# Kernel tuning notes

Hardware: AMD Instinct MI355X
Metric: run time of the kernel (lower is better)

## Reference

```python
import jax, jax.numpy as jnp
from jax import lax
import numpy as np

T, B, H, NUM_DATA, IN_DIM = 2048, 256, 128, 4096, 1


def setup_inputs() -> dict:
    key = jax.random.key(0)
    ks = jax.random.split(key, 9)
    s = 1.0 / np.sqrt(H)  # PyTorch LSTM/Linear default init scale
    inp = {
        "input": jax.random.normal(ks[0], (T, B, IN_DIM), dtype=jnp.float32),
        "label": jax.random.randint(ks[1], (B,), 0, NUM_DATA),
        "h0": jnp.zeros((1, NUM_DATA, H), dtype=jnp.float32),
        "W_ih": jax.random.uniform(ks[2], (4 * H, IN_DIM), jnp.float32, -s, s),
        "W_hh": jax.random.uniform(ks[3], (4 * H, H), jnp.float32, -s, s),
        "b_ih": jax.random.uniform(ks[4], (4 * H,), jnp.float32, -s, s),
        "b_hh": jax.random.uniform(ks[5], (4 * H,), jnp.float32, -s, s),
        "W_lin": jax.random.uniform(ks[6], (IN_DIM, H), jnp.float32, -s, s),
        "b_lin": jax.random.uniform(ks[7], (IN_DIM,), jnp.float32, -s, s),
    }
    return inp


def reference(input, label, h0, W_ih, W_hh, b_ih, b_hh, W_lin, b_lin):
    seq_len = input.shape[0]
    num_in_batch = input.shape[1]
    # Gather learned initial hidden state per sequence id (the python cat loop in torch)
    h = h0[0, label]                                   # (B, H)
    c = jnp.zeros_like(h)                              # (B, H)
    y0 = jnp.zeros((num_in_batch, IN_DIM), input.dtype)  # t=0 input is zeros
    b = b_ih + b_hh                                    # (4H,)

    def step(carry, _):
        h, c, x = carry
        gates = x @ W_ih.T + h @ W_hh.T + b            # (B, 4H); torch gate order i,f,g,o
        i, f, g, o = jnp.split(gates, 4, axis=-1)
        i = jax.nn.sigmoid(i)
        f = jax.nn.sigmoid(f)
        g = jnp.tanh(g)
        o = jax.nn.sigmoid(o)
        c = f * c + i * g
        h = o * jnp.tanh(c)
        y = h @ W_lin.T + b_lin                        # (B, 1) -> fed back as next input
        return (h, c, y), y

    _, ys = lax.scan(step, (h, c, y0), None, length=seq_len)
    return ys  # (T, B, 1), matches torch cat of (1, B, 1) along dim 0
```

## Files before the change

kernel.cpp:

```cpp
#include <hip/hip_runtime.h>
#include <math.h>

#define T_STEPS 2048
#define BATCH   256
#define HDIM    128

__device__ __forceinline__ float fast_rcp(float x) { return __builtin_amdgcn_rcpf(x); }
__device__ __forceinline__ float sigmoid_f(float x) { return fast_rcp(1.0f + __expf(-x)); }
__device__ __forceinline__ float tanh_f(float x) {
    float e = __expf(2.0f * x);
    return 1.0f - 2.0f * fast_rcp(e + 1.0f);
}

#define REP8(M) M(0) M(1) M(2) M(3) M(4) M(5) M(6) M(7)

__global__ __launch_bounds__(512, 2)
void lstm_seq_kernel(const int*   __restrict__ label,
                     const float* __restrict__ h0,
                     const float* __restrict__ W_ih,
                     const float* __restrict__ W_hh,
                     const float* __restrict__ b_ih,
                     const float* __restrict__ b_hh,
                     const float* __restrict__ W_lin,
                     const float* __restrict__ b_lin,
                     float*       __restrict__ out)
{
    const int tid   = threadIdx.x;
    const int batch = blockIdx.x;
    const int m     = tid >> 2;
    const int q     = tid & 3;
    const int q8    = q * 8;

    const int ri = m, rf = m + 128, rg = m + 256, ro = m + 384;

    __shared__ float hbuf[2][160];
    __shared__ __attribute__((aligned(16))) float hist[128 * 132];

    const float4* W4 = (const float4*)W_hh;
    const float4* L4 = (const float4*)W_lin;

    #define DECL_W(i) \
        float4 wi##i = W4[ri * 32 + q8 + (i)]; \
        float4 wf##i = W4[rf * 32 + q8 + (i)]; \
        float4 wg##i = W4[rg * 32 + q8 + (i)]; \
        float4 wo##i = W4[ro * 32 + q8 + (i)];
    REP8(DECL_W)

    const float wih_i = W_ih[ri], wih_f = W_ih[rf];
    const float wih_g = W_ih[rg], wih_o = W_ih[ro];
    const float blin  = b_lin[0];

    const float bi_ = b_ih[ri] + b_hh[ri] + wih_i * blin;
    const float bf_ = b_ih[rf] + b_hh[rf] + wih_f * blin;
    const float bg_ = b_ih[rg] + b_hh[rg] + wih_g * blin;
    const float bo_ = b_ih[ro] + b_hh[ro] + wih_o * blin;

    const float bi4_ = bi_ * 0.25f;
    const float bf4_ = bf_ * 0.25f;
    const float bg4_ = bg_ * 0.25f;
    const float bo4_ = bo_ * 0.25f;

    #define FOLD_W(i) { float4 lv = L4[q8 + (i)]; \
        wi##i.x = fmaf(wih_i, lv.x, wi##i.x); wi##i.y = fmaf(wih_i, lv.y, wi##i.y); \
        wi##i.z = fmaf(wih_i, lv.z, wi##i.z); wi##i.w = fmaf(wih_i, lv.w, wi##i.w); \
        wf##i.x = fmaf(wih_f, lv.x, wf##i.x); wf##i.y = fmaf(wih_f, lv.y, wf##i.y); \
        wf##i.z = fmaf(wih_f, lv.z, wf##i.z); wf##i.w = fmaf(wih_f, lv.w, wf##i.w); \
        wg##i.x = fmaf(wih_g, lv.x, wg##i.x); wg##i.y = fmaf(wih_g, lv.y, wg##i.y); \
        wg##i.z = fmaf(wih_g, lv.z, wg##i.z); wg##i.w = fmaf(wih_g, lv.w, wg##i.w); \
        wo##i.x = fmaf(wih_o, lv.x, wo##i.x); wo##i.y = fmaf(wih_o, lv.y, wo##i.y); \
        wo##i.z = fmaf(wih_o, lv.z, wo##i.z); wo##i.w = fmaf(wih_o, lv.w, wo##i.w); }
    REP8(FOLD_W)

    const int   lane = tid & 63;
    const int   ya0w = lane + ((lane >> 5) << 2);
    const float wl_a = W_lin[lane];
    const float wl_b = W_lin[lane + 64];
    const int   hword = m + ((m >> 5) << 2);

    if (tid < HDIM) hbuf[0][tid + ((tid >> 5) << 2)] = h0[label[batch] * HDIM + tid];
    __syncthreads();

    float p0 = hbuf[0][ya0w] * wl_a + hbuf[0][ya0w + 72] * wl_b;
    #pragma unroll
    for (int off = 1; off < 64; off <<= 1) p0 += __shfl_xor(p0, off, 64);
    const float y0 = p0 + blin;

    const float cbi = bi_ - wih_i * y0;
    const float cbf = bf_ - wih_f * y0;
    const float cbg = bg_ - wih_g * y0;
    const float cbo = bo_ - wih_o * y0;

    const float4* hq0 = (const float4*)(&hbuf[0][0] + 36 * q);
    float ai = 0.f, af = 0.f, ag = 0.f, ao = 0.f;
    #define DOT4(i) { float4 hv = hq0[(i)]; \
        ai = fmaf(hv.x, wi##i.x, ai); ai = fmaf(hv.y, wi##i.y, ai); \
        ai = fmaf(hv.z, wi##i.z, ai); ai = fmaf(hv.w, wi##i.w, ai); \
        af = fmaf(hv.x, wf##i.x, af); af = fmaf(hv.y, wf##i.y, af); \
        af = fmaf(hv.z, wf##i.z, af); af = fmaf(hv.w, wf##i.w, af); \
        ag = fmaf(hv.x, wg##i.x, ag); ag = fmaf(hv.y, wg##i.y, ag); \
        ag = fmaf(hv.z, wg##i.z, ag); ag = fmaf(hv.w, wg##i.w, ag); \
        ao = fmaf(hv.x, wo##i.x, ao); ao = fmaf(hv.y, wo##i.y, ao); \
        ao = fmaf(hv.z, wo##i.z, ao); ao = fmaf(hv.w, wo##i.w, ao); }
    REP8(DOT4)
    ai += __shfl_xor(ai, 1, 64); af += __shfl_xor(af, 1, 64);
    ag += __shfl_xor(ag, 1, 64); ao += __shfl_xor(ao, 1, 64);
    ai += __shfl_xor(ai, 2, 64); af += __shfl_xor(af, 2, 64);
    ag += __shfl_xor(ag, 2, 64); ao += __shfl_xor(ao, 2, 64);
    const float iv0 = sigmoid_f(ai + cbi);
    const float fv0 = sigmoid_f(af + cbf);
    const float gv0 = tanh_f  (ag + cbg);
    const float ov0 = sigmoid_f(ao + cbo);
    float c = iv0 * gv0;
    const float hn0 = ov0 * tanh_f(c);
    if (q == 0) { hbuf[1][hword] = hn0; hist[m] = hn0; }
    __syncthreads();

    const unsigned ldsA  = (unsigned)(unsigned long long)(&hbuf[0][0]);
    const unsigned histB = (unsigned)(unsigned long long)(&hist[0]);
    const unsigned vR0 = ldsA + 640u + 144u * (unsigned)q;
    const unsigned vW0 = ldsA + 4u * (unsigned)hword;
    const unsigned hW0 = histB + 528u + 4u * (unsigned)m;
    const unsigned fR0 = histB + 528u * (unsigned)m + 128u * (unsigned)q;
    const unsigned jO0 = 1024u * (unsigned)m;
    const unsigned vO0 = 4u * (unsigned)batch;
    const unsigned offI = (unsigned)(ri * 512 + q * 128);
    const unsigned offF = (unsigned)(rf * 512 + q * 128);
    const unsigned offG = (unsigned)(rg * 512 + q * 128);
    const unsigned offO = (unsigned)(ro * 512 + q * 128);
    const unsigned offL = (unsigned)(q * 128);

    asm volatile(
        "v_mov_b32 v220, %[bi]\n\t"
        "v_mov_b32 v221, 0\n\t"
        "v_mov_b32 v222, %[bf]\n\t"
        "v_mov_b32 v223, 0\n\t"
        "v_mov_b32 v224, %[bg]\n\t"
        "v_mov_b32 v225, 0\n\t"
        "v_mov_b32 v226, %[bo]\n\t"
        "v_mov_b32 v227, 0\n\t"
        "v_mov_b32 v185, %[blin]\n\t"
        "v_mov_b32 v168, %[c0]\n\t"
        "v_mov_b32 v172, %[vR]\n\t"
        "v_mov_b32 v173, %[vW]\n\t"
        "v_mov_b32 v174, %[hW]\n\t"
        "v_mov_b32 v184, %[fR]\n\t"
        "v_mov_b32 v171, %[jO]\n\t"
        "v_mov_b32 v176, %[vO]\n\t"
        "v_mov_b32 v175, 0xfffffd80\n\t"
        "v_and_b32 v170, 3, %[tid]\n\t"
        "v_cmp_eq_u32 vcc, 0, v170\n\t"
        "s_nop 4\n\t"
        "s_mov_b64 s[26:27], vcc\n\t"
        "global_load_dwordx4 v[32:35], %[offI], %[whh] offset:0\n\t"
        "global_load_dwordx4 v[36:39], %[offI], %[whh] offset:16\n\t"
        "global_load_dwordx4 v[40:43], %[offI], %[whh] offset:32\n\t"
        "global_load_dwordx4 v[44:47], %[offI], %[whh] offset:48\n\t"
        "global_load_dwordx4 v[48:51], %[offI], %[whh] offset:64\n\t"
        "global_load_dwordx4 v[52:55], %[offI], %[whh] offset:80\n\t"
        "global_load_dwordx4 v[56:59], %[offI], %[whh] offset:96\n\t"
        "global_load_dwordx4 v[60:63], %[offI], %[whh] offset:112\n\t"
        "global_load_dwordx4 v[64:67], %[offF], %[whh] offset:0\n\t"
        "global_load_dwordx4 v[68:71], %[offF], %[whh] offset:16\n\t"
        "global_load_dwordx4 v[72:75], %[offF], %[whh] offset:32\n\t"
        "global_load_dwordx4 v[76:79], %[offF], %[whh] offset:48\n\t"
        "global_load_dwordx4 v[80:83], %[offF], %[whh] offset:64\n\t"
        "global_load_dwordx4 v[84:87], %[offF], %[whh] offset:80\n\t"
        "global_load_dwordx4 v[88:91], %[offF], %[whh] offset:96\n\t"
        "global_load_dwordx4 v[92:95], %[offF], %[whh] offset:112\n\t"
        "global_load_dwordx4 v[96:99], %[offG], %[whh] offset:0\n\t"
        "global_load_dwordx4 v[100:103], %[offG], %[whh] offset:16\n\t"
        "global_load_dwordx4 v[104:107], %[offG], %[whh] offset:32\n\t"
        "global_load_dwordx4 v[108:111], %[offG], %[whh] offset:48\n\t"
        "global_load_dwordx4 v[112:115], %[offG], %[whh] offset:64\n\t"
        "global_load_dwordx4 v[116:119], %[offG], %[whh] offset:80\n\t"
        "global_load_dwordx4 v[120:123], %[offG], %[whh] offset:96\n\t"
        "global_load_dwordx4 v[124:127], %[offG], %[whh] offset:112\n\t"
        "global_load_dwordx4 v[128:131], %[offO], %[whh] offset:0\n\t"
        "global_load_dwordx4 v[132:135], %[offO], %[whh] offset:16\n\t"
        "global_load_dwordx4 v[136:139], %[offO], %[whh] offset:32\n\t"
        "global_load_dwordx4 v[140:143], %[offO], %[whh] offset:48\n\t"
        "global_load_dwordx4 v[144:147], %[offO], %[whh] offset:64\n\t"
        "global_load_dwordx4 v[148:151], %[offO], %[whh] offset:80\n\t"
        "global_load_dwordx4 v[152:155], %[offO], %[whh] offset:96\n\t"
        "global_load_dwordx4 v[156:159], %[offO], %[whh] offset:112\n\t"
        "global_load_dwordx4 v[188:191], %[offL], %[wlin] offset:0\n\t"
        "global_load_dwordx4 v[192:195], %[offL], %[wlin] offset:16\n\t"
        "global_load_dwordx4 v[196:199], %[offL], %[wlin] offset:32\n\t"
        "global_load_dwordx4 v[200:203], %[offL], %[wlin] offset:48\n\t"
        "global_load_dwordx4 v[204:207], %[offL], %[wlin] offset:64\n\t"
        "global_load_dwordx4 v[208:211], %[offL], %[wlin] offset:80\n\t"
        "global_load_dwordx4 v[212:215], %[offL], %[wlin] offset:96\n\t"
        "global_load_dwordx4 v[216:219], %[offL], %[wlin] offset:112\n\t"
        "s_waitcnt vmcnt(0)\n\t"
        ".set K_I, 0\n"
        ".rept 32\n"
        " v_fma_f32 v[32+K_I],  %[wihi], v[188+K_I], v[32+K_I]\n"
        " v_fma_f32 v[64+K_I],  %[wihf], v[188+K_I], v[64+K_I]\n"
        " v_fma_f32 v[96+K_I],  %[wihg], v[188+K_I], v[96+K_I]\n"
        " v_fma_f32 v[128+K_I], %[wiho], v[188+K_I], v[128+K_I]\n"
        " .set K_I, K_I+1\n"
        ".endr\n"
        "s_movk_i32 s24, 1\n\t"
        "1:\n\t"
        "ds_read_b128 v[0:3],   v172\n\t"
        "ds_read_b128 v[4:7],   v172 offset:16\n\t"
        "ds_read_b128 v[8:11],  v172 offset:32\n\t"
        "ds_read_b128 v[12:15], v172 offset:48\n\t"
        "ds_read_b128 v[16:19], v172 offset:64\n\t"
        "ds_read_b128 v[20:23], v172 offset:80\n\t"
        "ds_read_b128 v[24:27], v172 offset:96\n\t"
        "ds_read_b128 v[28:31], v172 offset:112\n\t"
        "s_waitcnt lgkmcnt(6)\n\t"
        "v_pk_fma_f32 v[160:161], v[0:1], v[32:33], v[220:221]\n\t"
        "v_pk_fma_f32 v[162:163], v[0:1], v[64:65], v[222:223]\n\t"
        "v_pk_fma_f32 v[164:165], v[0:1], v[96:97], v[224:225]\n\t"
        "v_pk_fma_f32 v[166:167], v[0:1], v[128:129], v[226:227]\n\t"
        ".set K_I, 2\n"
        ".rept 3\n"
        " v_pk_fma_f32 v[160:161], v[K_I:K_I+1], v[32+K_I:33+K_I], v[160:161]\n"
        " v_pk_fma_f32 v[162:163], v[K_I:K_I+1], v[64+K_I:65+K_I], v[162:163]\n"
        " v_pk_fma_f32 v[164:165], v[K_I:K_I+1], v[96+K_I:97+K_I], v[164:165]\n"
        " v_pk_fma_f32 v[166:167], v[K_I:K_I+1], v[128+K_I:129+K_I], v[166:167]\n"
        " .set K_I, K_I+2\n"
        ".endr\n"
        "s_waitcnt lgkmcnt(4)\n\t"
        ".rept 4\n"
        " v_pk_fma_f32 v[160:161], v[K_I:K_I+1], v[32+K_I:33+K_I], v[160:161]\n"
        " v_pk_fma_f32 v[162:163], v[K_I:K_I+1], v[64+K_I:65+K_I], v[162:163]\n"
        " v_pk_fma_f32 v[164:165], v[K_I:K_I+1], v[96+K_I:97+K_I], v[164:165]\n"
        " v_pk_fma_f32 v[166:167], v[K_I:K_I+1], v[128+K_I:129+K_I], v[166:167]\n"
        " .set K_I, K_I+2\n"
        ".endr\n"
        "s_waitcnt lgkmcnt(2)\n\t"
        ".rept 4\n"
        " v_pk_fma_f32 v[160:161], v[K_I:K_I+1], v[32+K_I:33+K_I], v[160:161]\n"
        " v_pk_fma_f32 v[162:163], v[K_I:K_I+1], v[64+K_I:65+K_I], v[162:163]\n"
        " v_pk_fma_f32 v[164:165], v[K_I:K_I+1], v[96+K_I:97+K_I], v[164:165]\n"
        " v_pk_fma_f32 v[166:167], v[K_I:K_I+1], v[128+K_I:129+K_I], v[166:167]\n"
        " .set K_I, K_I+2\n"
        ".endr\n"
        "s_waitcnt lgkmcnt(0)\n\t"
        ".rept 4\n"
        " v_pk_fma_f32 v[160:161], v[K_I:K_I+1], v[32+K_I:33+K_I], v[160:161]\n"
        " v_pk_fma_f32 v[162:163], v[K_I:K_I+1], v[64+K_I:65+K_I], v[162:163]\n"
        " v_pk_fma_f32 v[164:165], v[K_I:K_I+1], v[96+K_I:97+K_I], v[164:165]\n"
        " v_pk_fma_f32 v[166:167], v[K_I:K_I+1], v[128+K_I:129+K_I], v[166:167]\n"
        " .set K_I, K_I+2\n"
        ".endr\n"
        "v_add_f32 v160, v160, v161\n\t"
        "v_add_f32 v162, v162, v163\n\t"
        "v_add_f32 v164, v164, v165\n\t"
        "v_add_f32 v166, v166, v167\n\t"
        "v_add_f32_dpp v160, v160, v160 quad_perm:[1,0,3,2] row_mask:0xf bank_mask:0xf\n\t"
        "v_add_f32_dpp v162, v162, v162 quad_perm:[1,0,3,2] row_mask:0xf bank_mask:0xf\n\t"
        "v_add_f32_dpp v164, v164, v164 quad_perm:[1,0,3,2] row_mask:0xf bank_mask:0xf\n\t"
        "v_add_f32_dpp v166, v166, v166 quad_perm:[1,0,3,2] row_mask:0xf bank_mask:0xf\n\t"
        "v_add_f32_dpp v160, v160, v160 quad_perm:[2,3,0,1] row_mask:0xf bank_mask:0xf\n\t"
        "v_add_f32_dpp v162, v162, v162 quad_perm:[2,3,0,1] row_mask:0xf bank_mask:0xf\n\t"
        "v_add_f32_dpp v164, v164, v164 quad_perm:[2,3,0,1] row_mask:0xf bank_mask:0xf\n\t"
        "v_add_f32_dpp v166, v166, v166 quad_perm:[2,3,0,1] row_mask:0xf bank_mask:0xf\n\t"
        "v_mul_f32 v161, 0xbfb8aa3b, v160\n\t"
        "v_mul_f32 v163, 0xbfb8aa3b, v162\n\t"
        "v_mul_f32 v165, 0x4038aa3b, v164\n\t"
        "v_mul_f32 v167, 0xbfb8aa3b, v166\n\t"
        "v_exp_f32 v161, v161\n\t"
        "v_exp_f32 v163, v163\n\t"
        "v_exp_f32 v165, v165\n\t"
        "v_exp_f32 v167, v167\n\t"
        "v_add_f32 v161, 1.0, v161\n\t"
        "v_add_f32 v163, 1.0, v163\n\t"
        "v_add_f32 v165, 1.0, v165\n\t"
        "v_add_f32 v167, 1.0, v167\n\t"
        "v_rcp_f32 v165, v165\n\t"
        "v_rcp_f32 v160, v161\n\t"
        "v_rcp_f32 v162, v163\n\t"
        "v_rcp_f32 v166, v167\n\t"
        "v_fma_f32 v164, -2.0, v165, 1.0\n\t"
        "v_mul_f32 v170, v160, v164\n\t"
        "v_fma_f32 v168, v162, v168, v170\n\t"
        "v_mul_f32 v170, 0x4038aa3b, v168\n\t"
        "v_exp_f32 v170, v170\n\t"
        "s_nop 1\n\t"
        "v_add_f32 v170, 1.0, v170\n\t"
        "v_rcp_f32 v170, v170\n\t"
        "s_nop 1\n\t"
        "v_fma_f32 v169, -2.0, v170, 1.0\n\t"
        "v_mul_f32 v169, v166, v169\n\t"
        "s_mov_b64 s[22:23], exec\n\t"
        "s_mov_b64 exec, s[26:27]\n\t"
        "ds_write_b32 v173, v169\n\t"
        "ds_write_b32 v174, v169\n\t"
        "s_mov_b64 exec, s[22:23]\n\t"
        "v_add_u32 v172, v172, v175\n\t"
        "v_sub_u32 v173, v173, v175\n\t"
        "v_sub_u32 v175, 0, v175\n\t"
        "v_add_u32 v174, 0x210, v174\n\t"
        "s_waitcnt lgkmcnt(0)\n\t"
        "s_barrier\n\t"
        "s_and_b32 s20, s24, 127\n\t"
        "s_cmp_lg_u32 s20, 127\n\t"
        "s_cbranch_scc1 3f\n\t"
        "v_add_u32 v174, 0xfffef800, v174\n\t"
        "ds_read_b128 v[0:3],   v184\n\t"
        "ds_read_b128 v[4:7],   v184 offset:16\n\t"
        "ds_read_b128 v[8:11],  v184 offset:32\n\t"
        "ds_read_b128 v[12:15], v184 offset:48\n\t"
        "ds_read_b128 v[16:19], v184 offset:64\n\t"
        "ds_read_b128 v[20:23], v184 offset:80\n\t"
        "ds_read_b128 v[24:27], v184 offset:96\n\t"
        "ds_read_b128 v[28:31], v184 offset:112\n\t"
        "v_mov_b32 v164, 0\n\t"
        "s_waitcnt lgkmcnt(0)\n\t"
        ".set K_I, 0\n"
        ".rept 32\n"
        " v_fma_f32 v164, v[0+K_I], v[188+K_I], v164\n"
        " .set K_I, K_I+1\n"
        ".endr\n"
        "s_nop 1\n\t"
        "v_add_f32_dpp v164, v164, v164 quad_perm:[1,0,3,2] row_mask:0xf bank_mask:0xf\n\t"
        "s_nop 1\n\t"
        "v_add_f32_dpp v164, v164, v164 quad_perm:[2,3,0,1] row_mask:0xf bank_mask:0xf\n\t"
        "v_add_f32 v164, v164, v185\n\t"
        "v_add_u32 v170, v176, v171\n\t"
        "s_mov_b64 s[22:23], exec\n\t"
        "s_mov_b64 exec, s[26:27]\n\t"
        "global_store_dword v170, v164, %[outp]\n\t"
        "s_mov_b64 exec, s[22:23]\n\t"
        "v_add_u32 v176, 0x20000, v176\n\t"
        "s_barrier\n\t"
        "3:\n\t"
        "s_add_i32 s24, s24, 1\n\t"
        "s_cmp_lt_i32 s24, 2048\n\t"
        "s_cbranch_scc1 1b\n\t"
        :
        : [offI]"v"(offI), [offF]"v"(offF), [offG]"v"(offG), [offO]"v"(offO),
          [offL]"v"(offL), [whh]"s"(W_hh), [wlin]"s"(W_lin), [outp]"s"(out),
          [wihi]"v"(wih_i), [wihf]"v"(wih_f), [wihg]"v"(wih_g), [wiho]"v"(wih_o),
          [bi]"v"(bi4_), [bf]"v"(bf4_), [bg]"v"(bg4_), [bo]"v"(bo4_),
          [blin]"v"(blin), [c0]"v"(c),
          [vR]"v"(vR0), [vW]"v"(vW0), [hW]"v"(hW0), [fR]"v"(fR0),
          [jO]"v"(jO0), [vO]"v"(vO0), [tid]"v"(tid)
        : "memory", "scc", "vcc", "s20","s21","s22","s23","s24","s25","s26","s27",
          "v0","v1","v2","v3","v4","v5","v6","v7","v8","v9",
          "v10","v11","v12","v13","v14","v15","v16","v17","v18","v19",
          "v20","v21","v22","v23","v24","v25","v26","v27","v28","v29",
          "v30","v31","v32","v33","v34","v35","v36","v37","v38","v39",
          "v40","v41","v42","v43","v44","v45","v46","v47","v48","v49",
          "v50","v51","v52","v53","v54","v55","v56","v57","v58","v59",
          "v60","v61","v62","v63","v64","v65","v66","v67","v68","v69",
          "v70","v71","v72","v73","v74","v75","v76","v77","v78","v79",
          "v80","v81","v82","v83","v84","v85","v86","v87","v88","v89",
          "v90","v91","v92","v93","v94","v95","v96","v97","v98","v99",
          "v100","v101","v102","v103","v104","v105","v106","v107","v108","v109",
          "v110","v111","v112","v113","v114","v115","v116","v117","v118","v119",
          "v120","v121","v122","v123","v124","v125","v126","v127","v128","v129",
          "v130","v131","v132","v133","v134","v135","v136","v137","v138","v139",
          "v140","v141","v142","v143","v144","v145","v146","v147","v148","v149",
          "v150","v151","v152","v153","v154","v155","v156","v157","v158","v159",
          "v160","v161","v162","v163","v164","v165","v166","v167","v168","v169",
          "v170","v171","v172","v173","v174","v175","v176","v177","v178","v179",
          "v180","v181","v182","v183","v184","v185","v186","v187","v188","v189",
          "v190","v191","v192","v193","v194","v195","v196","v197","v198","v199",
          "v200","v201","v202","v203","v204","v205","v206","v207","v208","v209",
          "v210","v211","v212","v213","v214","v215","v216","v217","v218","v219",
          "v220","v221","v222","v223","v224","v225","v226","v227");
}

extern "C" void kernel_launch(void* const* d_in, const int* in_sizes, int n_in,
                              void* d_out, int out_size, void* d_ws, size_t ws_size,
                              hipStream_t stream) {
    const int*   label = (const int*)  d_in[1];
    const float* h0    = (const float*)d_in[2];
    const float* W_ih  = (const float*)d_in[3];
    const float* W_hh  = (const float*)d_in[4];
    const float* b_ih  = (const float*)d_in[5];
    const float* b_hh  = (const float*)d_in[6];
    const float* W_lin = (const float*)d_in[7];
    const float* b_lin = (const float*)d_in[8];
    float* out = (float*)d_out;

    lstm_seq_kernel<<<dim3(BATCH), dim3(512), 0, stream>>>(
        label, h0, W_ih, W_hh, b_ih, b_hh, W_lin, b_lin, out);
}
```

Before: 1.223 ms.

## Merge hidden-state ping-pong buffer into history ring and pack gate math

Drops the separate double-buffered hbuf. Each step now reads h directly from the previous slot of the padded history array (row stride 144) and writes the new h once instead of twice. This removes one LDS write per step plus some pointer bookkeeping from the serial critical path. The gate pre-activation scaling is also paired into v_pk_mul_f32 instructions on registers holding the log2e constants, cutting the scalar multiplies from four to two. The trade-off is a larger shared-memory footprint and dependence on correct wraparound offset arithmetic in hand-written asm.

```diff
diff --git a/kernel.cpp b/kernel.cpp
--- a/kernel.cpp
+++ b/kernel.cpp
@@ -33,8 +33,7 @@
 
     const int ri = m, rf = m + 128, rg = m + 256, ro = m + 384;
 
-    __shared__ float hbuf[2][160];
-    __shared__ __attribute__((aligned(16))) float hist[128 * 132];
+    __shared__ __attribute__((aligned(16))) float hist[128 * 144];
 
     const float4* W4 = (const float4*)W_hh;
     const float4* L4 = (const float4*)W_lin;
@@ -77,10 +76,11 @@
     const float wl_b = W_lin[lane + 64];
     const int   hword = m + ((m >> 5) << 2);
 
-    if (tid < HDIM) hbuf[0][tid + ((tid >> 5) << 2)] = h0[label[batch] * HDIM + tid];
+    float* slotI = &hist[144 * 127];
+    if (tid < HDIM) slotI[tid + ((tid >> 5) << 2)] = h0[label[batch] * HDIM + tid];
     __syncthreads();
 
-    float p0 = hbuf[0][ya0w] * wl_a + hbuf[0][ya0w + 72] * wl_b;
+    float p0 = slotI[ya0w] * wl_a + slotI[ya0w + 72] * wl_b;
     #pragma unroll
     for (int off = 1; off < 64; off <<= 1) p0 += __shfl_xor(p0, off, 64);
     const float y0 = p0 + blin;
@@ -90,7 +90,7 @@
     const float cbg = bg_ - wih_g * y0;
     const float cbo = bo_ - wih_o * y0;
 
-    const float4* hq0 = (const float4*)(&hbuf[0][0] + 36 * q);
+    const float4* hq0 = (const float4*)(slotI + 36 * q);
     float ai = 0.f, af = 0.f, ag = 0.f, ao = 0.f;
     #define DOT4(i) { float4 hv = hq0[(i)]; \
         ai = fmaf(hv.x, wi##i.x, ai); ai = fmaf(hv.y, wi##i.y, ai); \
@@ -112,15 +112,14 @@
     const float ov0 = sigmoid_f(ao + cbo);
     float c = iv0 * gv0;
     const float hn0 = ov0 * tanh_f(c);
-    if (q == 0) { hbuf[1][hword] = hn0; hist[m] = hn0; }
+    if (q == 0) hist[hword] = hn0;
     __syncthreads();
 
-    const unsigned ldsA  = (unsigned)(unsigned long long)(&hbuf[0][0]);
     const unsigned histB = (unsigned)(unsigned long long)(&hist[0]);
-    const unsigned vR0 = ldsA + 640u + 144u * (unsigned)q;
-    const unsigned vW0 = ldsA + 4u * (unsigned)hword;
-    const unsigned hW0 = histB + 528u + 4u * (unsigned)m;
-    const unsigned fR0 = histB + 528u * (unsigned)m + 128u * (unsigned)q;
+    const unsigned vR0 = histB + 144u * (unsigned)q;
+    const unsigned hW0 = histB + 576u + 4u * (unsigned)hword;
+    const unsigned vD0 = (unsigned)(-576 + 144 * q - 4 * hword);
+    const unsigned fR0 = histB + 576u * (unsigned)m + 144u * (unsigned)q;
     const unsigned jO0 = 1024u * (unsigned)m;
     const unsigned vO0 = 4u * (unsigned)batch;
     const unsigned offI = (unsigned)(ri * 512 + q * 128);
@@ -138,15 +137,18 @@
         "v_mov_b32 v225, 0\n\t"
         "v_mov_b32 v226, %[bo]\n\t"
         "v_mov_b32 v227, 0\n\t"
+        "v_mov_b32 v178, 0xbfb8aa3b\n\t"
+        "v_mov_b32 v179, 0xbfb8aa3b\n\t"
+        "v_mov_b32 v182, 0x4038aa3b\n\t"
+        "v_mov_b32 v183, 0xbfb8aa3b\n\t"
         "v_mov_b32 v185, %[blin]\n\t"
         "v_mov_b32 v168, %[c0]\n\t"
         "v_mov_b32 v172, %[vR]\n\t"
-        "v_mov_b32 v173, %[vW]\n\t"
         "v_mov_b32 v174, %[hW]\n\t"
+        "v_mov_b32 v186, %[vD]\n\t"
         "v_mov_b32 v184, %[fR]\n\t"
         "v_mov_b32 v171, %[jO]\n\t"
         "v_mov_b32 v176, %[vO]\n\t"
-        "v_mov_b32 v175, 0xfffffd80\n\t"
         "v_and_b32 v170, 3, %[tid]\n\t"
         "v_cmp_eq_u32 vcc, 0, v170\n\t"
         "s_nop 4\n\t"
@@ -248,36 +250,34 @@
         " .set K_I, K_I+2\n"
         ".endr\n"
         "v_add_f32 v160, v160, v161\n\t"
-        "v_add_f32 v162, v162, v163\n\t"
+        "v_add_f32 v161, v162, v163\n\t"
         "v_add_f32 v164, v164, v165\n\t"
-        "v_add_f32 v166, v166, v167\n\t"
+        "v_add_f32 v165, v166, v167\n\t"
         "v_add_f32_dpp v160, v160, v160 quad_perm:[1,0,3,2] row_mask:0xf bank_mask:0xf\n\t"
-        "v_add_f32_dpp v162, v162, v162 quad_perm:[1,0,3,2] row_mask:0xf bank_mask:0xf\n\t"
+        "v_add_f32_dpp v161, v161, v161 quad_perm:[1,0,3,2] row_mask:0xf bank_mask:0xf\n\t"
         "v_add_f32_dpp v164, v164, v164 quad_perm:[1,0,3,2] row_mask:0xf bank_mask:0xf\n\t"
-        "v_add_f32_dpp v166, v166, v166 quad_perm:[1,0,3,2] row_mask:0xf bank_mask:0xf\n\t"
+        "v_add_f32_dpp v165, v165, v165 quad_perm:[1,0,3,2] row_mask:0xf bank_mask:0xf\n\t"
         "v_add_f32_dpp v160, v160, v160 quad_perm:[2,3,0,1] row_mask:0xf bank_mask:0xf\n\t"
-        "v_add_f32_dpp v162, v162, v162 quad_perm:[2,3,0,1] row_mask:0xf bank_mask:0xf\n\t"
+        "v_add_f32_dpp v161, v161, v161 quad_perm:[2,3,0,1] row_mask:0xf bank_mask:0xf\n\t"
         "v_add_f32_dpp v164, v164, v164 quad_perm:[2,3,0,1] row_mask:0xf bank_mask:0xf\n\t"
-        "v_add_f32_dpp v166, v166, v166 quad_perm:[2,3,0,1] row_mask:0xf bank_mask:0xf\n\t"
-        "v_mul_f32 v161, 0xbfb8aa3b, v160\n\t"
-        "v_mul_f32 v163, 0xbfb8aa3b, v162\n\t"
-        "v_mul_f32 v165, 0x4038aa3b, v164\n\t"
-        "v_mul_f32 v167, 0xbfb8aa3b, v166\n\t"
-        "v_exp_f32 v161, v161\n\t"
+        "v_add_f32_dpp v165, v165, v165 quad_perm:[2,3,0,1] row_mask:0xf bank_mask:0xf\n\t"
+        "v_pk_mul_f32 v[162:163], v[178:179], v[160:161]\n\t"
+        "v_pk_mul_f32 v[166:167], v[182:183], v[164:165]\n\t"
+        "v_exp_f32 v162, v162\n\t"
         "v_exp_f32 v163, v163\n\t"
-        "v_exp_f32 v165, v165\n\t"
+        "v_exp_f32 v166, v166\n\t"
         "v_exp_f32 v167, v167\n\t"
-        "v_add_f32 v161, 1.0, v161\n\t"
+        "v_add_f32 v166, 1.0, v166\n\t"
+        "v_add_f32 v167, 1.0, v167\n\t"
+        "v_add_f32 v162, 1.0, v162\n\t"
         "v_add_f32 v163, 1.0, v163\n\t"
-        "v_add_f32 v165, 1.0, v165\n\t"
-        "v_add_f32 v167, 1.0, v167\n\t"
-        "v_rcp_f32 v165, v165\n\t"
-        "v_rcp_f32 v160, v161\n\t"
-        "v_rcp_f32 v162, v163\n\t"
-        "v_rcp_f32 v166, v167\n\t"
-        "v_fma_f32 v164, -2.0, v165, 1.0\n\t"
-        "v_mul_f32 v170, v160, v164\n\t"
-        "v_fma_f32 v168, v162, v168, v170\n\t"
+        "v_rcp_f32 v166, v166\n\t"
+        "v_rcp_f32 v162, v162\n\t"
+        "v_rcp_f32 v163, v163\n\t"
+        "v_rcp_f32 v167, v167\n\t"
+        "v_fma_f32 v164, -2.0, v166, 1.0\n\t"
+        "v_mul_f32 v170, v162, v164\n\t"
+        "v_fma_f32 v168, v163, v168, v170\n\t"
         "v_mul_f32 v170, 0x4038aa3b, v168\n\t"
         "v_exp_f32 v170, v170\n\t"
         "s_nop 1\n\t"
@@ -285,22 +285,19 @@
         "v_rcp_f32 v170, v170\n\t"
         "s_nop 1\n\t"
         "v_fma_f32 v169, -2.0, v170, 1.0\n\t"
-        "v_mul_f32 v169, v166, v169\n\t"
+        "v_mul_f32 v169, v167, v169\n\t"
         "s_mov_b64 s[22:23], exec\n\t"
         "s_mov_b64 exec, s[26:27]\n\t"
-        "ds_write_b32 v173, v169\n\t"
         "ds_write_b32 v174, v169\n\t"
         "s_mov_b64 exec, s[22:23]\n\t"
-        "v_add_u32 v172, v172, v175\n\t"
-        "v_sub_u32 v173, v173, v175\n\t"
-        "v_sub_u32 v175, 0, v175\n\t"
-        "v_add_u32 v174, 0x210, v174\n\t"
+        "v_add_u32 v174, 0x240, v174\n\t"
+        "v_add_u32 v172, v174, v186\n\t"
         "s_waitcnt lgkmcnt(0)\n\t"
         "s_barrier\n\t"
         "s_and_b32 s20, s24, 127\n\t"
         "s_cmp_lg_u32 s20, 127\n\t"
         "s_cbranch_scc1 3f\n\t"
-        "v_add_u32 v174, 0xfffef800, v174\n\t"
+        "v_add_u32 v174, 0xfffee000, v174\n\t"
         "ds_read_b128 v[0:3],   v184\n\t"
         "ds_read_b128 v[4:7],   v184 offset:16\n\t"
         "ds_read_b128 v[8:11],  v184 offset:32\n\t"
@@ -338,7 +335,7 @@
           [wihi]"v"(wih_i), [wihf]"v"(wih_f), [wihg]"v"(wih_g), [wiho]"v"(wih_o),
           [bi]"v"(bi4_), [bf]"v"(bf4_), [bg]"v"(bg4_), [bo]"v"(bo4_),
           [blin]"v"(blin), [c0]"v"(c),
-          [vR]"v"(vR0), [vW]"v"(vW0), [hW]"v"(hW0), [fR]"v"(fR0),
+          [vR]"v"(vR0), [hW]"v"(hW0), [vD]"v"(vD0), [fR]"v"(fR0),
           [jO]"v"(jO0), [vO]"v"(vO0), [tid]"v"(tid)
         : "memory", "scc", "vcc", "s20","s21","s22","s23","s24","s25","s26","s27",
           "v0","v1","v2","v3","v4","v5","v6","v7","v8","v9",
```

New measurement: 1.191 ms. -2.5%, faster.
